# Optimization experiments

Hardware: AMD Instinct MI355X
Metric: run time of the kernel (lower is better)

Reference implementation:

```python
import jax, jax.numpy as jnp
import numpy as np

GRID_SIZE = 5
SPLINE_ORDER = 3
NUM_COEFF = GRID_SIZE + SPLINE_ORDER  # 8
L = 3
B, I, H = 4096, 256, 512
EPS = 1e-5


def make_grid(in_features):
    # efficient-kan default grid over [-1, 1] extended by spline_order knots each side
    h = 2.0 / GRID_SIZE
    g = jnp.arange(-SPLINE_ORDER, GRID_SIZE + SPLINE_ORDER + 1, dtype=jnp.float32) * h - 1.0
    return jnp.broadcast_to(g, (in_features, g.shape[0]))  # (in, G+2k+1)


def b_splines(x, grid):
    # x: (B, in), grid: (in, G+2k+1) -> (B, in, G+k) via Cox-de-Boor recursion
    xg = x[..., None]
    bases = ((xg >= grid[:, :-1]) & (xg < grid[:, 1:])).astype(x.dtype)
    for j in range(1, SPLINE_ORDER + 1):
        left = (xg - grid[:, :-(j + 1)]) / (grid[:, j:-1] - grid[:, :-(j + 1)])
        right = (grid[:, j + 1:] - xg) / (grid[:, j + 1:] - grid[:, 1:-j])
        bases = left * bases[..., :-1] + right * bases[..., 1:]
    return bases


def kan_linear(x, base_w, spline_w, grid):
    # base path: SiLU(x) @ W_base^T ; spline path: sum over (in, coeff)
    base = jax.nn.silu(x) @ base_w.T
    spl = jnp.einsum('bik,oik->bo', b_splines(x, grid), spline_w)
    return base + spl


def layer_norm(x, g, b):
    mu = jnp.mean(x, axis=-1, keepdims=True)
    var = jnp.var(x, axis=-1, keepdims=True)
    return (x - mu) / jnp.sqrt(var + EPS) * g + b


def _sublayer(z_prev, wx_b, wx_s, wh_b, wh_s, hz_b, hz_s, phi_b, phi_s,
              hh_w, hh_b, ln_g, ln_b, x_t, grid_in, grid_h):
    s_t = kan_linear(x_t, wx_b, wx_s, grid_in) + kan_linear(z_prev, wh_b, wh_s, grid_h)
    o_t = kan_linear(s_t, phi_b, phi_s, grid_h)
    z_t = layer_norm(z_prev @ hh_w.T + hh_b + kan_linear(o_t, hz_b, hz_s, grid_h), ln_g, ln_b)
    return o_t, z_t


def setup_inputs() -> dict:
    key = jax.random.key(0)
    ks = jax.random.split(key, 24)
    s = 0.05  # small init to keep gates/splines in sane range
    inp = {
        'x_t': jax.random.normal(ks[0], (B, I), jnp.float32),
        'h_prev': jax.random.normal(ks[1], (B, H), jnp.float32),
        'c_prev': jax.random.normal(ks[2], (B, H), jnp.float32),
        'z_prev': jax.random.normal(ks[3], (L, B, H), jnp.float32),
        'wx_base': jax.random.normal(ks[4], (L, H, I), jnp.float32) * s,
        'wx_spline': jax.random.normal(ks[5], (L, H, I, NUM_COEFF), jnp.float32) * s,
        'wh_base': jax.random.normal(ks[6], (L, H, H), jnp.float32) * s,
        'wh_spline': jax.random.normal(ks[7], (L, H, H, NUM_COEFF), jnp.float32) * s,
        'hz_base': jax.random.normal(ks[8], (L, H, H), jnp.float32) * s,
        'hz_spline': jax.random.normal(ks[9], (L, H, H, NUM_COEFF), jnp.float32) * s,
        'phi_base': jax.random.normal(ks[10], (L, H, H), jnp.float32) * s,
        'phi_spline': jax.random.normal(ks[11], (L, H, H, NUM_COEFF), jnp.float32) * s,
        'hh_w': jax.random.normal(ks[12], (L, H, H), jnp.float32) * s,
        'hh_b': jax.random.normal(ks[13], (L, H), jnp.float32) * s,
        'ln_g': jnp.ones((L, H), jnp.float32),
        'ln_b': jnp.zeros((L, H), jnp.float32),
        'f_w': jax.random.normal(ks[14], (H, I + H), jnp.float32) * s,
        'f_b': jax.random.normal(ks[15], (H,), jnp.float32) * s,
        'i_w': jax.random.normal(ks[16], (H, I + H), jnp.float32) * s,
        'i_b': jax.random.normal(ks[17], (H,), jnp.float32) * s,
        'g_w': jax.random.normal(ks[18], (H, I + H), jnp.float32) * s,
        'g_b': jax.random.normal(ks[19], (H,), jnp.float32) * s,
        'o_w': jax.random.normal(ks[20], (H, L * H), jnp.float32) * s,
        'o_b': jax.random.normal(ks[21], (H,), jnp.float32) * s,
    }
    return inp


def reference(x_t, h_prev, c_prev, z_prev, wx_base, wx_spline, wh_base, wh_spline,
              hz_base, hz_spline, phi_base, phi_spline, hh_w, hh_b, ln_g, ln_b,
              f_w, f_b, i_w, i_b, g_w, g_b, o_w, o_b):
    grid_in = make_grid(I)
    grid_h = make_grid(H)
    cat = jnp.concatenate([x_t, h_prev], axis=-1)  # (B, I+H)
    f_t = jax.nn.sigmoid(cat @ f_w.T + f_b)
    i_t = jax.nn.sigmoid(cat @ i_w.T + i_b)
    g_t = jnp.tanh(cat @ g_w.T + g_b)
    # vmap the RKAN sublayer over the L stacked sublayers
    sub = jax.vmap(_sublayer, in_axes=(0,) * 13 + (None, None, None))
    o_all, z_all = sub(z_prev, wx_base, wx_spline, wh_base, wh_spline,
                       hz_base, hz_spline, phi_base, phi_spline,
                       hh_w, hh_b, ln_g, ln_b, x_t, grid_in, grid_h)
    # concat sublayer phi outputs: (L,B,H) -> (B, L*H)
    r_t = jnp.transpose(o_all, (1, 0, 2)).reshape(B, L * H)
    o_t = jax.nn.sigmoid(r_t @ o_w.T + o_b)
    c_t = f_t * c_prev + i_t * g_t
    h_t = o_t * jnp.tanh(c_t)
    return h_t, c_t, z_all
```

## Files before the change

### kernel.cpp

```cpp
#include <hip/hip_runtime.h>

typedef __attribute__((ext_vector_type(8))) short short8;
typedef __attribute__((ext_vector_type(4))) short short4v;
typedef __attribute__((ext_vector_type(4))) float floatx4;

__device__ inline short f2bf(float v) {
    unsigned u = __builtin_bit_cast(unsigned, v);
    unsigned r = (u + 0x7fffu + ((u >> 16) & 1u)) >> 16;
    return (short)r;
}
__device__ inline float bf2f(short s) {
    unsigned u = ((unsigned)(unsigned short)s) << 16;
    return __builtin_bit_cast(float, u);
}
__device__ inline short4v pack4(float4 v) {
    short4v o;
    o[0] = f2bf(v.x); o[1] = f2bf(v.y); o[2] = f2bf(v.z); o[3] = f2bf(v.w);
    return o;
}
__device__ inline short4v silu4(float4 v) {
    float4 s;
    s.x = v.x / (1.f + __expf(-v.x));
    s.y = v.y / (1.f + __expf(-v.y));
    s.z = v.z / (1.f + __expf(-v.z));
    s.w = v.w / (1.f + __expf(-v.w));
    return pack4(s);
}

__device__ inline void spline8(float v, short* arr) {
    float u = (v + 2.2f) * 2.5f;
    float fj = floorf(u);
    int jj = (int)fj;
    float t1 = u - fj;
    float ok = (jj >= 0 && jj <= 10) ? (1.f / 6.f) : 0.f;
    float t2 = t1 * t1, t3 = t2 * t1;
    float omt = 1.f - t1;
    short sw0 = f2bf(omt * omt * omt * ok);
    short sw1 = f2bf((3.f * t3 - 6.f * t2 + 4.f) * ok);
    short sw2 = f2bf((-3.f * t3 + 3.f * t2 + 3.f * t1 + 1.f) * ok);
    short sw3 = f2bf(t3 * ok);
#pragma unroll
    for (int s = 0; s < 8; ++s) {
        int rr = s - jj + 3;
        arr[s] = (rr == 0) ? sw0 : (rr == 1) ? sw1 : (rr == 2) ? sw2
                 : (rr == 3) ? sw3 : (short)0;
    }
}
__device__ inline void expand4(float4 v, short* silu_dst, short* spl_dst) {
    *(short4v*)silu_dst = silu4(v);
    short arr[8];
    spline8(v.x, arr); *(short8*)(spl_dst)      = *(const short8*)arr;
    spline8(v.y, arr); *(short8*)(spl_dst + 8)  = *(const short8*)arr;
    spline8(v.z, arr); *(short8*)(spl_dst + 16) = *(const short8*)arr;
    spline8(v.w, arr); *(short8*)(spl_dst + 24) = *(const short8*)arr;
}

__global__ __launch_bounds__(256, 3) void gemm128(
    int S, int Kh,
    const short* __restrict__ A0, int lda0, long sA0, int K0,
    const short* __restrict__ W0, int ldw0, long sW0,
    const short* __restrict__ A1, int lda1, long sA1, int K1,
    const short* __restrict__ W1, int ldw1, long sW1,
    float* __restrict__ C, int ldc, long sC, long sSplit)
{
    __shared__ short As[128 * 64];
    __shared__ short Ws[128 * 64];
    const int t = threadIdx.x;
    int n = blockIdx.x + (blockIdx.y << 5) + (blockIdx.z << 7);
    int k8 = n & 7, j = n >> 3;
    int byi = j & 3;
    int t2 = j >> 2;
    int bxi = k8 * 4 + (t2 & 3);
    int bzi = t2 >> 2;
    const int z = bzi / S, s = bzi % S;
    const int bm = bxi * 128, bn = byi * 128;
    const int lane = t & 63, w = t >> 6;
    const int wm = (w >> 1) * 64, wn = (w & 1) * 64;
    const int lrow = lane & 15, quad = lane >> 4;

    floatx4 acc[4][4] = {};

    const int kbeg = s * Kh, kend = kbeg + Kh;

    const short* A = A0 + (long)z * sA0;
    const short* W = W0 + (long)z * sW0;
    int lda = lda0, ldw = ldw0;
    int kb = kbeg, ke = (kend < K0) ? kend : K0;

    for (int seg = 0; seg < 2; ++seg) {
        for (int kv = kb; kv < ke; kv += 64) {
#pragma unroll
            for (int i = 0; i < 4; ++i) {
                int c = i * 256 + t;
                int row = c >> 3;
                int cg = ((c ^ row) & 7) * 8;
                const short* gp = A + (long)(bm + row) * lda + kv + cg;
                __builtin_amdgcn_global_load_lds(
                    (const __attribute__((address_space(1))) void*)gp,
                    (__attribute__((address_space(3))) void*)(As + c * 8), 16, 0, 0);
                const short* gq = W + (long)(bn + row) * ldw + kv + cg;
                __builtin_amdgcn_global_load_lds(
                    (const __attribute__((address_space(1))) void*)gq,
                    (__attribute__((address_space(3))) void*)(Ws + c * 8), 16, 0, 0);
            }
            __syncthreads();
#pragma unroll
            for (int kk = 0; kk < 2; ++kk) {
                short8 af[4], bfr[4];
#pragma unroll
                for (int mi = 0; mi < 4; ++mi) {
                    int r = wm + mi * 16 + lrow;
                    af[mi] = *(const short8*)(As + r * 64 +
                                              (((kk * 4 + quad) ^ (r & 7)) * 8));
                }
#pragma unroll
                for (int ni = 0; ni < 4; ++ni) {
                    int r = wn + ni * 16 + lrow;
                    bfr[ni] = *(const short8*)(Ws + r * 64 +
                                               (((kk * 4 + quad) ^ (r & 7)) * 8));
                }
#pragma unroll
                for (int mi = 0; mi < 4; ++mi)
#pragma unroll
                    for (int ni = 0; ni < 4; ++ni)
                        acc[mi][ni] = __builtin_amdgcn_mfma_f32_16x16x32_bf16(
                            af[mi], bfr[ni], acc[mi][ni], 0, 0, 0);
            }
            __syncthreads();
        }
        A = A1 + (long)z * sA1;
        W = W1 + (long)z * sW1;
        lda = lda1; ldw = ldw1;
        kb = ((kbeg > K0) ? kbeg : K0) - K0;
        ke = kend - K0;
    }

    float* Cz = C + (long)z * sC + (long)s * sSplit;
#pragma unroll
    for (int mi = 0; mi < 4; ++mi)
#pragma unroll
        for (int ni = 0; ni < 4; ++ni)
#pragma unroll
            for (int r = 0; r < 4; ++r) {
                int row = bm + wm + mi * 16 + quad * 4 + r;
                int col = bn + wn + ni * 16 + lrow;
                Cz[(long)row * ldc + col] = acc[mi][ni][r];
            }
}

__global__ __launch_bounds__(256) void gemm64(
    const short* __restrict__ A0, int lda0, long sA0, int K0,
    const short* __restrict__ W0, int ldw0, long sW0,
    short* __restrict__ C, int ldc, long sC)
{
    __shared__ short As[64 * 64];
    __shared__ short Ws[128 * 64];
    const int t = threadIdx.x;
    const int z = blockIdx.z;
    const int bm = blockIdx.x * 64;
    const int bn = blockIdx.y * 128;
    const int lane = t & 63, w = t >> 6;
    const int wm = (w >> 1) * 32, wn = (w & 1) * 64;
    const int lrow = lane & 15, quad = lane >> 4;

    floatx4 acc[2][4] = {};

    const short* A = A0 + (long)z * sA0;
    const short* W = W0 + (long)z * sW0;

    for (int k0 = 0; k0 < K0; k0 += 64) {
#pragma unroll
        for (int i = 0; i < 2; ++i) {
            int c = i * 256 + t;
            int row = c >> 3;
            int cg = ((c ^ row) & 7) * 8;
            const short* gp = A + (long)(bm + row) * lda0 + k0 + cg;
            __builtin_amdgcn_global_load_lds(
                (const __attribute__((address_space(1))) void*)gp,
                (__attribute__((address_space(3))) void*)(As + c * 8), 16, 0, 0);
        }
#pragma unroll
        for (int i = 0; i < 4; ++i) {
            int c = i * 256 + t;
            int row = c >> 3;
            int cg = ((c ^ row) & 7) * 8;
            const short* gq = W + (long)(bn + row) * ldw0 + k0 + cg;
            __builtin_amdgcn_global_load_lds(
                (const __attribute__((address_space(1))) void*)gq,
                (__attribute__((address_space(3))) void*)(Ws + c * 8), 16, 0, 0);
        }
        __syncthreads();
#pragma unroll
        for (int kk = 0; kk < 2; ++kk) {
            short8 af[2], bfr[4];
#pragma unroll
            for (int mi = 0; mi < 2; ++mi) {
                int r = wm + mi * 16 + lrow;
                af[mi] = *(const short8*)(As + r * 64 +
                                          (((kk * 4 + quad) ^ (r & 7)) * 8));
            }
#pragma unroll
            for (int ni = 0; ni < 4; ++ni) {
                int r = wn + ni * 16 + lrow;
                bfr[ni] = *(const short8*)(Ws + r * 64 +
                                           (((kk * 4 + quad) ^ (r & 7)) * 8));
            }
#pragma unroll
            for (int mi = 0; mi < 2; ++mi)
#pragma unroll
                for (int ni = 0; ni < 4; ++ni)
                    acc[mi][ni] = __builtin_amdgcn_mfma_f32_16x16x32_bf16(
                        af[mi], bfr[ni], acc[mi][ni], 0, 0, 0);
        }
        __syncthreads();
    }

    short* Cz = C + (long)z * sC;
#pragma unroll
    for (int mi = 0; mi < 2; ++mi)
#pragma unroll
        for (int ni = 0; ni < 4; ++ni)
#pragma unroll
            for (int r = 0; r < 4; ++r) {
                int row = bm + wm + mi * 16 + quad * 4 + r;
                int col = bn + wn + ni * 16 + lrow;
                Cz[(long)row * ldc + col] = f2bf(acc[mi][ni][r]);
            }
}

__global__ __launch_bounds__(256) void megapack8(
    const float* __restrict__ wx_b, const float* __restrict__ wx_s,
    const float* __restrict__ wh_b, const float* __restrict__ wh_s,
    const float* __restrict__ hz_b, const float* __restrict__ hz_s,
    const float* __restrict__ phi_b, const float* __restrict__ phi_s,
    const float* __restrict__ hh_w, const float* __restrict__ o_w,
    const float* __restrict__ f_w, const float* __restrict__ i_w,
    const float* __restrict__ g_w,
    short* __restrict__ Wx, short* __restrict__ Wh, short* __restrict__ Whz,
    short* __restrict__ Wphi, short* __restrict__ HHb, short* __restrict__ OWb,
    short* __restrict__ Wg)
{
    int bid = blockIdx.x, tid = threadIdx.x;
    const float* sp;
    short* dst;
    long e;
    if (bid < 1728) {
        e = ((long)bid * 256 + tid) * 8;
        int r = (int)(e / 2304), c = (int)(e % 2304);
        sp = (c < 256) ? wx_b + (long)r * 256 + c
                       : wx_s + (long)r * 2048 + (c - 256);
        dst = Wx + e;
    } else if (bid < 12096) {
        int jb = bid - 1728;
        int job = jb / 3456, lb = jb % 3456;
        const float* bp = (job == 0) ? wh_b : (job == 1) ? hz_b : phi_b;
        const float* spw = (job == 0) ? wh_s : (job == 1) ? hz_s : phi_s;
        short* dp = (job == 0) ? Wh : (job == 1) ? Whz : Wphi;
        e = ((long)lb * 256 + tid) * 8;
        int r = (int)(e / 4608), c = (int)(e % 4608);
        sp = (c < 512) ? bp + (long)r * 512 + c
                       : spw + (long)r * 4096 + (c - 512);
        dst = dp + e;
    } else if (bid < 12480) {
        e = ((long)(bid - 12096) * 256 + tid) * 8;
        sp = hh_w + e; dst = HHb + e;
    } else if (bid < 12864) {
        e = ((long)(bid - 12480) * 256 + tid) * 8;
        sp = o_w + e; dst = OWb + e;
    } else if (bid < 13056) {
        e = ((long)(bid - 12864) * 256 + tid) * 8;
        sp = f_w + e; dst = Wg + e;
    } else if (bid < 13248) {
        e = ((long)(bid - 13056) * 256 + tid) * 8;
        sp = i_w + e; dst = Wg + 393216 + e;
    } else {
        e = ((long)(bid - 13248) * 256 + tid) * 8;
        sp = g_w + e; dst = Wg + 786432 + e;
    }
    float4 a = *(const float4*)sp;
    float4 b = *(const float4*)(sp + 4);
    short8 o;
    o[0] = f2bf(a.x); o[1] = f2bf(a.y); o[2] = f2bf(a.z); o[3] = f2bf(a.w);
    o[4] = f2bf(b.x); o[5] = f2bf(b.y); o[6] = f2bf(b.z); o[7] = f2bf(b.w);
    *(short8*)dst = o;
}

__global__ __launch_bounds__(256) void prep_acts4(
    const float* __restrict__ x_t, const float* __restrict__ h_prev,
    const float* __restrict__ z_prev,
    short* __restrict__ Xe, short* __restrict__ Agate,
    short* __restrict__ Ze, short* __restrict__ zraw)
{
    int bid = blockIdx.x, tid = threadIdx.x;
    if (bid < 1024) {
        int r = (bid << 2) + (tid >> 6);
        int i = (tid & 63) << 2;
        float4 v = *(const float4*)(x_t + (long)r * 256 + i);
        *(short4v*)(Agate + (long)r * 768 + i) = pack4(v);
        long ob = (long)r * 2304;
        expand4(v, Xe + ob + i, Xe + ob + 256 + (long)i * 8);
    } else if (bid < 3072) {
        long idx = ((long)(bid - 1024) * 256 + tid) * 4;
        float4 v = *(const float4*)(h_prev + idx);
        long b = idx >> 9; int hh = (int)(idx & 511);
        *(short4v*)(Agate + b * 768 + 256 + hh) = pack4(v);
    } else {
        int j = bid - 3072;
        int r = (j << 1) + (tid >> 7);
        int i = (tid & 127) << 2;
        float4 v = *(const float4*)(z_prev + (long)r * 512 + i);
        *(short4v*)(zraw + (long)r * 512 + i) = pack4(v);
        long ob = (long)r * 4608;
        expand4(v, Ze + ob + i, Ze + ob + 512 + (long)i * 8);
    }
}

__global__ __launch_bounds__(256) void expand_pair4(
    const float* __restrict__ P, long sSplit, int S,
    short* __restrict__ out, short* __restrict__ compact)
{
    int tid = threadIdx.x;
    int r = (blockIdx.x << 1) + (tid >> 7);
    int i = (tid & 127) << 2;
    long idx = (long)r * 512 + i;
    float4 v = *(const float4*)(P + idx);
    for (int s = 1; s < S; ++s) {
        float4 a = *(const float4*)(P + idx + (long)s * sSplit);
        v.x += a.x; v.y += a.y; v.z += a.z; v.w += a.w;
    }
    if (compact) *(short4v*)(compact + idx) = pack4(v);
    long ob = (long)r * 4608;
    expand4(v, out + ob + i, out + ob + 512 + (long)i * 8);
}

__global__ __launch_bounds__(256) void ln_wave(const float* __restrict__ P,
                                               long sSplit, int S,
                                               const float* __restrict__ hh_b,
                                               const float* __restrict__ ln_g,
                                               const float* __restrict__ ln_b,
                                               float* __restrict__ out)
{
    int wv = threadIdx.x >> 6, lane = threadIdx.x & 63;
    int row = blockIdx.x * 4 + wv;
    int l = row >> 12;
    int col = lane * 8;
    long base = (long)row * 512 + col;
    float v[8];
#pragma unroll
    for (int e = 0; e < 8; ++e) v[e] = hh_b[l * 512 + col + e];
    for (int s = 0; s < S; ++s) {
        float4 a = *(const float4*)(P + base + (long)s * sSplit);
        float4 b = *(const float4*)(P + base + 4 + (long)s * sSplit);
        v[0] += a.x; v[1] += a.y; v[2] += a.z; v[3] += a.w;
        v[4] += b.x; v[5] += b.y; v[6] += b.z; v[7] += b.w;
    }
    float sm = 0.f, sq = 0.f;
#pragma unroll
    for (int e = 0; e < 8; ++e) { sm += v[e]; sq += v[e] * v[e]; }
#pragma unroll
    for (int off = 32; off; off >>= 1) {
        sm += __shfl_down(sm, off);
        sq += __shfl_down(sq, off);
    }
    sm = __shfl(sm, 0);
    sq = __shfl(sq, 0);
    float mu = sm * (1.f / 512.f);
    float var = sq * (1.f / 512.f) - mu * mu;
    float rstd = rsqrtf(var + 1e-5f);
    float o[8];
#pragma unroll
    for (int e = 0; e < 8; ++e)
        o[e] = (v[e] - mu) * rstd * ln_g[l * 512 + col + e] + ln_b[l * 512 + col + e];
    float* op = out + base;
    *(float4*)op = make_float4(o[0], o[1], o[2], o[3]);
    *(float4*)(op + 4) = make_float4(o[4], o[5], o[6], o[7]);
}

__global__ __launch_bounds__(256) void cell_epilogue(const short* __restrict__ gates,
                                                     const short* __restrict__ opre,
                                                     const float* __restrict__ c_prev,
                                                     const float* __restrict__ f_b,
                                                     const float* __restrict__ i_b,
                                                     const float* __restrict__ g_b,
                                                     const float* __restrict__ o_b,
                                                     float* __restrict__ out)
{
    long idx = blockIdx.x * 256L + threadIdx.x;
    long b = idx >> 9; int h = (int)(idx & 511);
    const short* g = gates + b * 1536;
    float fp = bf2f(g[h]) + f_b[h];
    float ip = bf2f(g[512 + h]) + i_b[h];
    float gp = bf2f(g[1024 + h]) + g_b[h];
    float op = bf2f(opre[idx]) + o_b[h];
    float ft = 1.f / (1.f + __expf(-fp));
    float it = 1.f / (1.f + __expf(-ip));
    float gt = tanhf(gp);
    float ot = 1.f / (1.f + __expf(-op));
    float c = ft * c_prev[idx] + it * gt;
    out[idx] = ot * tanhf(c);
    out[idx + 2097152] = c;
}

extern "C" void kernel_launch(void* const* d_in, const int* in_sizes, int n_in,
                              void* d_out, int out_size, void* d_ws, size_t ws_size,
                              hipStream_t stream)
{
    const float* x_t       = (const float*)d_in[0];
    const float* h_prev    = (const float*)d_in[1];
    const float* c_prev    = (const float*)d_in[2];
    const float* z_prev    = (const float*)d_in[3];
    const float* wx_base   = (const float*)d_in[4];
    const float* wx_spline = (const float*)d_in[5];
    const float* wh_base   = (const float*)d_in[6];
    const float* wh_spline = (const float*)d_in[7];
    const float* hz_base   = (const float*)d_in[8];
    const float* hz_spline = (const float*)d_in[9];
    const float* phi_base  = (const float*)d_in[10];
    const float* phi_spline= (const float*)d_in[11];
    const float* hh_w      = (const float*)d_in[12];
    const float* hh_b      = (const float*)d_in[13];
    const float* ln_g      = (const float*)d_in[14];
    const float* ln_b      = (const float*)d_in[15];
    const float* f_w       = (const float*)d_in[16];
    const float* f_b       = (const float*)d_in[17];
    const float* i_w       = (const float*)d_in[18];
    const float* i_b       = (const float*)d_in[19];
    const float* g_w       = (const float*)d_in[20];
    const float* g_b       = (const float*)d_in[21];
    const float* o_w       = (const float*)d_in[22];
    const float* o_b       = (const float*)d_in[23];
    float* out = (float*)d_out;
    const long BH = 4096L * 512;

    char* p = (char*)d_ws;
    auto alloc = [&](size_t bytes) {
        char* q = p;
        p += (bytes + 255) & ~(size_t)255;
        return q;
    };

    short* Wx   = (short*)alloc(3L * 512 * 2304 * 2);
    short* Wh   = (short*)alloc(3L * 512 * 4608 * 2);
    short* Whz  = (short*)alloc(3L * 512 * 4608 * 2);
    short* Wphi = (short*)alloc(3L * 512 * 4608 * 2);
    short* HHb  = (short*)alloc(3L * 512 * 512 * 2);
    short* OWb  = (short*)alloc(512L * 1536 * 2);
    short* Wg   = (short*)alloc(1536L * 768 * 2);
    short* Agate= (short*)alloc(4096L * 768 * 2);
    short* zraw = (short*)alloc(3L * 4096 * 512 * 2);
    short* XR   = (short*)alloc(4096L * 2304 * 2);
    short* Ebuf = (short*)alloc(3L * 4096 * 4608 * 2);

    const int S = 2;
    const long PS = 3L * 4096 * 512;
    float* Pbuf = (float*)alloc((size_t)S * PS * 4);

    short* Xe = XR;
    short* Rbuf = XR;
    short* gbuf = Ebuf;
    short* opre = Ebuf + 4096L * 1536;

    megapack8<<<13440, 256, 0, stream>>>(
        wx_base, wx_spline, wh_base, wh_spline, hz_base, hz_spline,
        phi_base, phi_spline, hh_w, o_w, f_w, i_w, g_w,
        Wx, Wh, Whz, Wphi, HHb, OWb, Wg);

    prep_acts4<<<9216, 256, 0, stream>>>(x_t, h_prev, z_prev, Xe, Agate, Ebuf, zraw);

    gemm128<<<dim3(32, 4, 3 * S), 256, 0, stream>>>(S, 3456,
        Xe, 2304, 0, 2304,                 Wx, 2304, 512L * 2304,
        Ebuf, 4608, 4096L * 4608, 4608,    Wh, 4608, 512L * 4608,
        Pbuf, 512, 4096L * 512, PS);

    expand_pair4<<<6144, 256, 0, stream>>>(Pbuf, PS, S, Ebuf, (short*)0);

    gemm128<<<dim3(32, 4, 3 * S), 256, 0, stream>>>(S, 2304,
        Ebuf, 4608, 4096L * 4608, 4608,    Wphi, 4608, 512L * 4608,
        zraw, 0, 0, 0,                     Wphi, 0, 0,
        Pbuf, 1536, 512, PS);

    expand_pair4<<<6144, 256, 0, stream>>>(Pbuf, PS, S, Ebuf, Rbuf);

    gemm128<<<dim3(32, 4, 3 * S), 256, 0, stream>>>(S, 2560,
        Ebuf, 13824, 4608, 4608,           Whz, 4608, 512L * 4608,
        zraw, 512, 4096L * 512, 512,       HHb, 512, 512L * 512,
        Pbuf, 512, 4096L * 512, PS);

    ln_wave<<<3072, 256, 0, stream>>>(Pbuf, PS, S, hh_b, ln_g, ln_b, out + 2 * BH);

    gemm64<<<dim3(64, 12, 1), 256, 0, stream>>>(
        Agate, 768, 0, 768,  Wg, 768, 0,
        gbuf, 1536, 0);

    gemm64<<<dim3(64, 4, 1), 256, 0, stream>>>(
        Rbuf, 1536, 0, 1536, OWb, 1536, 0,
        opre, 512, 0);

    cell_epilogue<<<8192, 256, 0, stream>>>(gbuf, opre, c_prev, f_b, i_b, g_b, o_b, out);
}
```

Measured before the change: 705.3 us.

## Triple-buffer GEMM K-loop with async LDS loads and unify GEMM kernels

```diff
diff --git a/kernel.cpp b/kernel.cpp
--- a/kernel.cpp
+++ b/kernel.cpp
@@ -55,177 +55,133 @@
     spline8(v.w, arr); *(short8*)(spl_dst + 24) = *(const short8*)arr;
 }
 
-__global__ __launch_bounds__(256, 3) void gemm128(
-    int S, int Kh,
+__global__ __launch_bounds__(256, 3) void gemmp(
+    int nbx, int nby, int S, int Kh,
     const short* __restrict__ A0, int lda0, long sA0, int K0,
     const short* __restrict__ W0, int ldw0, long sW0,
-    const short* __restrict__ A1, int lda1, long sA1, int K1,
+    const short* __restrict__ A1, int lda1, long sA1,
     const short* __restrict__ W1, int ldw1, long sW1,
-    float* __restrict__ C, int ldc, long sC, long sSplit)
-{
-    __shared__ short As[128 * 64];
-    __shared__ short Ws[128 * 64];
+    float* __restrict__ C, short* __restrict__ Cb,
+    int ldc, long sC, long sSplit)
+{
+    __shared__ short As[3 * 128 * 32];
+    __shared__ short Ws[3 * 128 * 32];
     const int t = threadIdx.x;
-    int n = blockIdx.x + (blockIdx.y << 5) + (blockIdx.z << 7);
+    const int n = blockIdx.x;
     int k8 = n & 7, j = n >> 3;
-    int byi = j & 3;
-    int t2 = j >> 2;
-    int bxi = k8 * 4 + (t2 & 3);
-    int bzi = t2 >> 2;
+    int byi = j % nby;
+    int j2 = j / nby;
+    int mper = nbx >> 3;
+    int bxi = k8 * mper + (j2 % mper);
+    int bzi = j2 / mper;
     const int z = bzi / S, s = bzi % S;
     const int bm = bxi * 128, bn = byi * 128;
     const int lane = t & 63, w = t >> 6;
     const int wm = (w >> 1) * 64, wn = (w & 1) * 64;
     const int lrow = lane & 15, quad = lane >> 4;
 
+    const short* A0z = A0 + (long)z * sA0;
+    const short* W0z = W0 + (long)z * sW0;
+    const short* A1z = A1 + (long)z * sA1;
+    const short* W1z = W1 + (long)z * sW1;
+    const int kbeg = s * Kh;
+    const int nsteps = Kh >> 5;
+
     floatx4 acc[4][4] = {};
 
-    const int kbeg = s * Kh, kend = kbeg + Kh;
-
-    const short* A = A0 + (long)z * sA0;
-    const short* W = W0 + (long)z * sW0;
-    int lda = lda0, ldw = ldw0;
-    int kb = kbeg, ke = (kend < K0) ? kend : K0;
-
-    for (int seg = 0; seg < 2; ++seg) {
-        for (int kv = kb; kv < ke; kv += 64) {
-#pragma unroll
-            for (int i = 0; i < 4; ++i) {
-                int c = i * 256 + t;
-                int row = c >> 3;
-                int cg = ((c ^ row) & 7) * 8;
-                const short* gp = A + (long)(bm + row) * lda + kv + cg;
-                __builtin_amdgcn_global_load_lds(
-                    (const __attribute__((address_space(1))) void*)gp,
-                    (__attribute__((address_space(3))) void*)(As + c * 8), 16, 0, 0);
-                const short* gq = W + (long)(bn + row) * ldw + kv + cg;
-                __builtin_amdgcn_global_load_lds(
-                    (const __attribute__((address_space(1))) void*)gq,
-                    (__attribute__((address_space(3))) void*)(Ws + c * 8), 16, 0, 0);
-            }
-            __syncthreads();
-#pragma unroll
-            for (int kk = 0; kk < 2; ++kk) {
-                short8 af[4], bfr[4];
-#pragma unroll
-                for (int mi = 0; mi < 4; ++mi) {
-                    int r = wm + mi * 16 + lrow;
-                    af[mi] = *(const short8*)(As + r * 64 +
-                                              (((kk * 4 + quad) ^ (r & 7)) * 8));
-                }
-#pragma unroll
-                for (int ni = 0; ni < 4; ++ni) {
-                    int r = wn + ni * 16 + lrow;
-                    bfr[ni] = *(const short8*)(Ws + r * 64 +
-                                               (((kk * 4 + quad) ^ (r & 7)) * 8));
-                }
-#pragma unroll
-                for (int mi = 0; mi < 4; ++mi)
-#pragma unroll
-                    for (int ni = 0; ni < 4; ++ni)
-                        acc[mi][ni] = __builtin_amdgcn_mfma_f32_16x16x32_bf16(
-                            af[mi], bfr[ni], acc[mi][ni], 0, 0, 0);
-            }
-            __syncthreads();
-        }
-        A = A1 + (long)z * sA1;
-        W = W1 + (long)z * sW1;
-        lda = lda1; ldw = ldw1;
-        kb = ((kbeg > K0) ? kbeg : K0) - K0;
-        ke = kend - K0;
-    }
-
-    float* Cz = C + (long)z * sC + (long)s * sSplit;
-#pragma unroll
-    for (int mi = 0; mi < 4; ++mi)
-#pragma unroll
-        for (int ni = 0; ni < 4; ++ni)
-#pragma unroll
-            for (int r = 0; r < 4; ++r) {
-                int row = bm + wm + mi * 16 + quad * 4 + r;
-                int col = bn + wn + ni * 16 + lrow;
-                Cz[(long)row * ldc + col] = acc[mi][ni][r];
-            }
-}
-
-__global__ __launch_bounds__(256) void gemm64(
-    const short* __restrict__ A0, int lda0, long sA0, int K0,
-    const short* __restrict__ W0, int ldw0, long sW0,
-    short* __restrict__ C, int ldc, long sC)
-{
-    __shared__ short As[64 * 64];
-    __shared__ short Ws[128 * 64];
-    const int t = threadIdx.x;
-    const int z = blockIdx.z;
-    const int bm = blockIdx.x * 64;
-    const int bn = blockIdx.y * 128;
-    const int lane = t & 63, w = t >> 6;
-    const int wm = (w >> 1) * 32, wn = (w & 1) * 64;
-    const int lrow = lane & 15, quad = lane >> 4;
-
-    floatx4 acc[2][4] = {};
-
-    const short* A = A0 + (long)z * sA0;
-    const short* W = W0 + (long)z * sW0;
-
-    for (int k0 = 0; k0 < K0; k0 += 64) {
+    auto stage = [&](int b, int step) {
+        int kv = kbeg + (step << 5);
+        const short *Ab, *Wb;
+        int la, lw;
+        if (kv < K0) { Ab = A0z + kv; la = lda0; Wb = W0z + kv; lw = ldw0; }
+        else         { Ab = A1z + (kv - K0); la = lda1; Wb = W1z + (kv - K0); lw = ldw1; }
+        short* Ad = As + b * 4096;
+        short* Wd = Ws + b * 4096;
 #pragma unroll
         for (int i = 0; i < 2; ++i) {
             int c = i * 256 + t;
-            int row = c >> 3;
-            int cg = ((c ^ row) & 7) * 8;
-            const short* gp = A + (long)(bm + row) * lda0 + k0 + cg;
+            int row = c >> 2;
+            int cg = ((c ^ row) & 3) * 8;
+            const short* gp = Ab + (long)(bm + row) * la + cg;
             __builtin_amdgcn_global_load_lds(
                 (const __attribute__((address_space(1))) void*)gp,
-                (__attribute__((address_space(3))) void*)(As + c * 8), 16, 0, 0);
-        }
-#pragma unroll
-        for (int i = 0; i < 4; ++i) {
-            int c = i * 256 + t;
-            int row = c >> 3;
-            int cg = ((c ^ row) & 7) * 8;
-            const short* gq = W + (long)(bn + row) * ldw0 + k0 + cg;
+                (__attribute__((address_space(3))) void*)(Ad + c * 8), 16, 0, 0);
+            const short* gq = Wb + (long)(bn + row) * lw + cg;
             __builtin_amdgcn_global_load_lds(
                 (const __attribute__((address_space(1))) void*)gq,
-                (__attribute__((address_space(3))) void*)(Ws + c * 8), 16, 0, 0);
+                (__attribute__((address_space(3))) void*)(Wd + c * 8), 16, 0, 0);
         }
-        __syncthreads();
-#pragma unroll
-        for (int kk = 0; kk < 2; ++kk) {
-            short8 af[2], bfr[4];
-#pragma unroll
-            for (int mi = 0; mi < 2; ++mi) {
-                int r = wm + mi * 16 + lrow;
-                af[mi] = *(const short8*)(As + r * 64 +
-                                          (((kk * 4 + quad) ^ (r & 7)) * 8));
-            }
-#pragma unroll
-            for (int ni = 0; ni < 4; ++ni) {
-                int r = wn + ni * 16 + lrow;
-                bfr[ni] = *(const short8*)(Ws + r * 64 +
-                                           (((kk * 4 + quad) ^ (r & 7)) * 8));
-            }
-#pragma unroll
-            for (int mi = 0; mi < 2; ++mi)
-#pragma unroll
-                for (int ni = 0; ni < 4; ++ni)
-                    acc[mi][ni] = __builtin_amdgcn_mfma_f32_16x16x32_bf16(
-                        af[mi], bfr[ni], acc[mi][ni], 0, 0, 0);
+    };
+
+    stage(0, 0);
+    stage(1, 1);
+
+    int cur = 0;
+    for (int st = 0; st < nsteps; ++st) {
+        int rem = nsteps - st;
+        if (rem > 2) {
+            int tsel = cur + 2; if (tsel >= 3) tsel -= 3;
+            stage(tsel, st + 2);
+            asm volatile("s_waitcnt vmcnt(8)" ::: "memory");
+        } else if (rem == 2) {
+            asm volatile("s_waitcnt vmcnt(4)" ::: "memory");
+        } else {
+            asm volatile("s_waitcnt vmcnt(0)" ::: "memory");
         }
-        __syncthreads();
-    }
-
-    short* Cz = C + (long)z * sC;
-#pragma unroll
-    for (int mi = 0; mi < 2; ++mi)
-#pragma unroll
-        for (int ni = 0; ni < 4; ++ni)
-#pragma unroll
-            for (int r = 0; r < 4; ++r) {
-                int row = bm + wm + mi * 16 + quad * 4 + r;
-                int col = bn + wn + ni * 16 + lrow;
-                Cz[(long)row * ldc + col] = f2bf(acc[mi][ni][r]);
-            }
+        __builtin_amdgcn_s_barrier();
+        __builtin_amdgcn_sched_barrier(0);
+
+        const short* Ab = As + cur * 4096;
+        const short* Wb = Ws + cur * 4096;
+        short8 af[4], bfr[4];
+#pragma unroll
+        for (int mi = 0; mi < 4; ++mi) {
+            int r = wm + mi * 16 + lrow;
+            af[mi] = *(const short8*)(Ab + r * 32 + ((quad ^ (r & 3)) * 8));
+        }
+#pragma unroll
+        for (int ni = 0; ni < 4; ++ni) {
+            int r = wn + ni * 16 + lrow;
+            bfr[ni] = *(const short8*)(Wb + r * 32 + ((quad ^ (r & 3)) * 8));
+        }
+#pragma unroll
+        for (int mi = 0; mi < 4; ++mi)
+#pragma unroll
+            for (int ni = 0; ni < 4; ++ni)
+                acc[mi][ni] = __builtin_amdgcn_mfma_f32_16x16x32_bf16(
+                    af[mi], bfr[ni], acc[mi][ni], 0, 0, 0);
+
+        asm volatile("s_waitcnt lgkmcnt(0)" ::: "memory");
+        __builtin_amdgcn_sched_barrier(0);
+        __builtin_amdgcn_s_barrier();
+        cur = (cur == 2) ? 0 : cur + 1;
+    }
+
+    if (C) {
+        float* Cz = C + (long)z * sC + (long)s * sSplit;
+#pragma unroll
+        for (int mi = 0; mi < 4; ++mi)
+#pragma unroll
+            for (int ni = 0; ni < 4; ++ni)
+#pragma unroll
+                for (int r = 0; r < 4; ++r) {
+                    int row = bm + wm + mi * 16 + quad * 4 + r;
+                    int col = bn + wn + ni * 16 + lrow;
+                    Cz[(long)row * ldc + col] = acc[mi][ni][r];
+                }
+    } else {
+        short* Cz = Cb + (long)z * sC;
+#pragma unroll
+        for (int mi = 0; mi < 4; ++mi)
+#pragma unroll
+            for (int ni = 0; ni < 4; ++ni)
+#pragma unroll
+                for (int r = 0; r < 4; ++r) {
+                    int row = bm + wm + mi * 16 + quad * 4 + r;
+                    int col = bn + wn + ni * 16 + lrow;
+                    Cz[(long)row * ldc + col] = f2bf(acc[mi][ni][r]);
+                }
+    }
 }
 
 __global__ __launch_bounds__(256) void megapack8(
@@ -305,8 +261,8 @@
         long b = idx >> 9; int hh = (int)(idx & 511);
         *(short4v*)(Agate + b * 768 + 256 + hh) = pack4(v);
     } else {
-        int j = bid - 3072;
-        int r = (j << 1) + (tid >> 7);
+        int jz = bid - 3072;
+        int r = (jz << 1) + (tid >> 7);
         int i = (tid & 127) << 2;
         float4 v = *(const float4*)(z_prev + (long)r * 512 + i);
         *(short4v*)(zraw + (long)r * 512 + i) = pack4(v);
@@ -467,34 +423,36 @@
 
     prep_acts4<<<9216, 256, 0, stream>>>(x_t, h_prev, z_prev, Xe, Agate, Ebuf, zraw);
 
-    gemm128<<<dim3(32, 4, 3 * S), 256, 0, stream>>>(S, 3456,
-        Xe, 2304, 0, 2304,                 Wx, 2304, 512L * 2304,
-        Ebuf, 4608, 4096L * 4608, 4608,    Wh, 4608, 512L * 4608,
-        Pbuf, 512, 4096L * 512, PS);
+    gemmp<<<768, 256, 0, stream>>>(32, 4, 2, 3456,
+        Xe, 2304, 0L, 2304,              Wx, 2304, 512L * 2304,
+        Ebuf, 4608, 4096L * 4608,        Wh, 4608, 512L * 4608,
+        Pbuf, (short*)0, 512, 4096L * 512, PS);
 
     expand_pair4<<<6144, 256, 0, stream>>>(Pbuf, PS, S, Ebuf, (short*)0);
 
-    gemm128<<<dim3(32, 4, 3 * S), 256, 0, stream>>>(S, 2304,
-        Ebuf, 4608, 4096L * 4608, 4608,    Wphi, 4608, 512L * 4608,
-        zraw, 0, 0, 0,                     Wphi, 0, 0,
-        Pbuf, 1536, 512, PS);
+    gemmp<<<768, 256, 0, stream>>>(32, 4, 2, 2304,
+        Ebuf, 4608, 4096L * 4608, 4608,  Wphi, 4608, 512L * 4608,
+        Ebuf, 4608, 4096L * 4608,        Wphi, 4608, 512L * 4608,
+        Pbuf, (short*)0, 1536, 512, PS);
 
     expand_pair4<<<6144, 256, 0, stream>>>(Pbuf, PS, S, Ebuf, Rbuf);
 
-    gemm128<<<dim3(32, 4, 3 * S), 256, 0, stream>>>(S, 2560,
-        Ebuf, 13824, 4608, 4608,           Whz, 4608, 512L * 4608,
-        zraw, 512, 4096L * 512, 512,       HHb, 512, 512L * 512,
-        Pbuf, 512, 4096L * 512, PS);
+    gemmp<<<768, 256, 0, stream>>>(32, 4, 2, 2560,
+        Ebuf, 13824, 4608, 4608,         Whz, 4608, 512L * 4608,
+        zraw, 512, 4096L * 512,          HHb, 512, 512L * 512,
+        Pbuf, (short*)0, 512, 4096L * 512, PS);
 
     ln_wave<<<3072, 256, 0, stream>>>(Pbuf, PS, S, hh_b, ln_g, ln_b, out + 2 * BH);
 
-    gemm64<<<dim3(64, 12, 1), 256, 0, stream>>>(
-        Agate, 768, 0, 768,  Wg, 768, 0,
-        gbuf, 1536, 0);
-
-    gemm64<<<dim3(64, 4, 1), 256, 0, stream>>>(
-        Rbuf, 1536, 0, 1536, OWb, 1536, 0,
-        opre, 512, 0);
+    gemmp<<<384, 256, 0, stream>>>(32, 12, 1, 768,
+        Agate, 768, 0L, 768,             Wg, 768, 0L,
+        Agate, 768, 0L,                  Wg, 768, 0L,
+        (float*)0, gbuf, 1536, 0, 0);
+
+    gemmp<<<128, 256, 0, stream>>>(32, 4, 1, 1536,
+        Rbuf, 1536, 0L, 1536,            OWb, 1536, 0L,
+        Rbuf, 1536, 0L,                  OWb, 1536, 0L,
+        (float*)0, opre, 512, 0, 0);
 
     cell_epilogue<<<8192, 256, 0, stream>>>(gbuf, opre, c_prev, f_b, i_b, g_b, o_b, out);
 }
```

New measurement: 754.8 us. 7.0% more time.

## Load GEMM weight fragments directly from global into registers, dropping LDS staging

Applied to the files above, without the earlier changes.

```diff
diff --git a/kernel.cpp b/kernel.cpp
--- a/kernel.cpp
+++ b/kernel.cpp
@@ -55,16 +55,15 @@
     spline8(v.w, arr); *(short8*)(spl_dst + 24) = *(const short8*)arr;
 }
 
-__global__ __launch_bounds__(256, 3) void gemm128(
+__global__ __launch_bounds__(256, 4) void gemm128w(
     int S, int Kh,
     const short* __restrict__ A0, int lda0, long sA0, int K0,
     const short* __restrict__ W0, int ldw0, long sW0,
-    const short* __restrict__ A1, int lda1, long sA1, int K1,
+    const short* __restrict__ A1, int lda1, long sA1,
     const short* __restrict__ W1, int ldw1, long sW1,
     float* __restrict__ C, int ldc, long sC, long sSplit)
 {
     __shared__ short As[128 * 64];
-    __shared__ short Ws[128 * 64];
     const int t = threadIdx.x;
     int n = blockIdx.x + (blockIdx.y << 5) + (blockIdx.z << 7);
     int k8 = n & 7, j = n >> 3;
@@ -88,6 +87,7 @@
     int kb = kbeg, ke = (kend < K0) ? kend : K0;
 
     for (int seg = 0; seg < 2; ++seg) {
+        const short* Wb0 = W + (long)(bn + wn + lrow) * ldw;
         for (int kv = kb; kv < ke; kv += 64) {
 #pragma unroll
             for (int i = 0; i < 4; ++i) {
@@ -98,15 +98,18 @@
                 __builtin_amdgcn_global_load_lds(
                     (const __attribute__((address_space(1))) void*)gp,
                     (__attribute__((address_space(3))) void*)(As + c * 8), 16, 0, 0);
-                const short* gq = W + (long)(bn + row) * ldw + kv + cg;
-                __builtin_amdgcn_global_load_lds(
-                    (const __attribute__((address_space(1))) void*)gq,
-                    (__attribute__((address_space(3))) void*)(Ws + c * 8), 16, 0, 0);
             }
+            short8 bfr[2][4];
+#pragma unroll
+            for (int kk = 0; kk < 2; ++kk)
+#pragma unroll
+                for (int ni = 0; ni < 4; ++ni)
+                    bfr[kk][ni] = *(const short8*)(
+                        Wb0 + (long)ni * 16 * ldw + kv + (kk * 4 + quad) * 8);
             __syncthreads();
 #pragma unroll
             for (int kk = 0; kk < 2; ++kk) {
-                short8 af[4], bfr[4];
+                short8 af[4];
 #pragma unroll
                 for (int mi = 0; mi < 4; ++mi) {
                     int r = wm + mi * 16 + lrow;
@@ -114,17 +117,11 @@
                                               (((kk * 4 + quad) ^ (r & 7)) * 8));
                 }
 #pragma unroll
-                for (int ni = 0; ni < 4; ++ni) {
-                    int r = wn + ni * 16 + lrow;
-                    bfr[ni] = *(const short8*)(Ws + r * 64 +
-                                               (((kk * 4 + quad) ^ (r & 7)) * 8));
-                }
-#pragma unroll
                 for (int mi = 0; mi < 4; ++mi)
 #pragma unroll
                     for (int ni = 0; ni < 4; ++ni)
                         acc[mi][ni] = __builtin_amdgcn_mfma_f32_16x16x32_bf16(
-                            af[mi], bfr[ni], acc[mi][ni], 0, 0, 0);
+                            af[mi], bfr[kk][ni], acc[mi][ni], 0, 0, 0);
             }
             __syncthreads();
         }
@@ -148,13 +145,12 @@
             }
 }
 
-__global__ __launch_bounds__(256) void gemm64(
+__global__ __launch_bounds__(256, 4) void gemm64w(
     const short* __restrict__ A0, int lda0, long sA0, int K0,
     const short* __restrict__ W0, int ldw0, long sW0,
     short* __restrict__ C, int ldc, long sC)
 {
     __shared__ short As[64 * 64];
-    __shared__ short Ws[128 * 64];
     const int t = threadIdx.x;
     const int z = blockIdx.z;
     const int bm = blockIdx.x * 64;
@@ -167,6 +163,7 @@
 
     const short* A = A0 + (long)z * sA0;
     const short* W = W0 + (long)z * sW0;
+    const short* Wb0 = W + (long)(bn + wn + lrow) * ldw0;
 
     for (int k0 = 0; k0 < K0; k0 += 64) {
 #pragma unroll
@@ -179,20 +176,17 @@
                 (const __attribute__((address_space(1))) void*)gp,
                 (__attribute__((address_space(3))) void*)(As + c * 8), 16, 0, 0);
         }
-#pragma unroll
-        for (int i = 0; i < 4; ++i) {
-            int c = i * 256 + t;
-            int row = c >> 3;
-            int cg = ((c ^ row) & 7) * 8;
-            const short* gq = W + (long)(bn + row) * ldw0 + k0 + cg;
-            __builtin_amdgcn_global_load_lds(
-                (const __attribute__((address_space(1))) void*)gq,
-                (__attribute__((address_space(3))) void*)(Ws + c * 8), 16, 0, 0);
-        }
+        short8 bfr[2][4];
+#pragma unroll
+        for (int kk = 0; kk < 2; ++kk)
+#pragma unroll
+            for (int ni = 0; ni < 4; ++ni)
+                bfr[kk][ni] = *(const short8*)(
+                    Wb0 + (long)ni * 16 * ldw0 + k0 + (kk * 4 + quad) * 8);
         __syncthreads();
 #pragma unroll
         for (int kk = 0; kk < 2; ++kk) {
-            short8 af[2], bfr[4];
+            short8 af[2];
 #pragma unroll
             for (int mi = 0; mi < 2; ++mi) {
                 int r = wm + mi * 16 + lrow;
@@ -200,17 +194,11 @@
                                           (((kk * 4 + quad) ^ (r & 7)) * 8));
             }
 #pragma unroll
-            for (int ni = 0; ni < 4; ++ni) {
-                int r = wn + ni * 16 + lrow;
-                bfr[ni] = *(const short8*)(Ws + r * 64 +
-                                           (((kk * 4 + quad) ^ (r & 7)) * 8));
-            }
-#pragma unroll
             for (int mi = 0; mi < 2; ++mi)
 #pragma unroll
                 for (int ni = 0; ni < 4; ++ni)
                     acc[mi][ni] = __builtin_amdgcn_mfma_f32_16x16x32_bf16(
-                        af[mi], bfr[ni], acc[mi][ni], 0, 0, 0);
+                        af[mi], bfr[kk][ni], acc[mi][ni], 0, 0, 0);
         }
         __syncthreads();
     }
@@ -305,8 +293,8 @@
         long b = idx >> 9; int hh = (int)(idx & 511);
         *(short4v*)(Agate + b * 768 + 256 + hh) = pack4(v);
     } else {
-        int j = bid - 3072;
-        int r = (j << 1) + (tid >> 7);
+        int jz = bid - 3072;
+        int r = (jz << 1) + (tid >> 7);
         int i = (tid & 127) << 2;
         float4 v = *(const float4*)(z_prev + (long)r * 512 + i);
         *(short4v*)(zraw + (long)r * 512 + i) = pack4(v);
@@ -467,33 +455,33 @@
 
     prep_acts4<<<9216, 256, 0, stream>>>(x_t, h_prev, z_prev, Xe, Agate, Ebuf, zraw);
 
-    gemm128<<<dim3(32, 4, 3 * S), 256, 0, stream>>>(S, 3456,
-        Xe, 2304, 0, 2304,                 Wx, 2304, 512L * 2304,
-        Ebuf, 4608, 4096L * 4608, 4608,    Wh, 4608, 512L * 4608,
+    gemm128w<<<dim3(32, 4, 3 * S), 256, 0, stream>>>(S, 3456,
+        Xe, 2304, 0L, 2304,              Wx, 2304, 512L * 2304,
+        Ebuf, 4608, 4096L * 4608,        Wh, 4608, 512L * 4608,
         Pbuf, 512, 4096L * 512, PS);
 
     expand_pair4<<<6144, 256, 0, stream>>>(Pbuf, PS, S, Ebuf, (short*)0);
 
-    gemm128<<<dim3(32, 4, 3 * S), 256, 0, stream>>>(S, 2304,
-        Ebuf, 4608, 4096L * 4608, 4608,    Wphi, 4608, 512L * 4608,
-        zraw, 0, 0, 0,                     Wphi, 0, 0,
+    gemm128w<<<dim3(32, 4, 3 * S), 256, 0, stream>>>(S, 2304,
+        Ebuf, 4608, 4096L * 4608, 4608,  Wphi, 4608, 512L * 4608,
+        Ebuf, 4608, 4096L * 4608,        Wphi, 4608, 512L * 4608,
         Pbuf, 1536, 512, PS);
 
     expand_pair4<<<6144, 256, 0, stream>>>(Pbuf, PS, S, Ebuf, Rbuf);
 
-    gemm128<<<dim3(32, 4, 3 * S), 256, 0, stream>>>(S, 2560,
-        Ebuf, 13824, 4608, 4608,           Whz, 4608, 512L * 4608,
-        zraw, 512, 4096L * 512, 512,       HHb, 512, 512L * 512,
+    gemm128w<<<dim3(32, 4, 3 * S), 256, 0, stream>>>(S, 2560,
+        Ebuf, 13824, 4608, 4608,         Whz, 4608, 512L * 4608,
+        zraw, 512, 4096L * 512,          HHb, 512, 512L * 512,
         Pbuf, 512, 4096L * 512, PS);
 
     ln_wave<<<3072, 256, 0, stream>>>(Pbuf, PS, S, hh_b, ln_g, ln_b, out + 2 * BH);
 
-    gemm64<<<dim3(64, 12, 1), 256, 0, stream>>>(
-        Agate, 768, 0, 768,  Wg, 768, 0,
+    gemm64w<<<dim3(64, 12, 1), 256, 0, stream>>>(
+        Agate, 768, 0L, 768,  Wg, 768, 0L,
         gbuf, 1536, 0);
 
-    gemm64<<<dim3(64, 4, 1), 256, 0, stream>>>(
-        Rbuf, 1536, 0, 1536, OWb, 1536, 0,
+    gemm64w<<<dim3(64, 4, 1), 256, 0, stream>>>(
+        Rbuf, 1536, 0L, 1536, OWb, 1536, 0L,
         opre, 512, 0);
 
     cell_epilogue<<<8192, 256, 0, stream>>>(gbuf, opre, c_prev, f_b, i_b, g_b, o_b, out);
```

New measurement: 975.4 us. +38.3%, slower.
